# Performance work log

Hardware: AMD Instinct MI355X
Metric: run time of the kernel (lower is better)

## Reference

```python
import jax, jax.numpy as jnp
import numpy as np

B, L, N, F = 8, 4096, 128, 128          # batch, pixels (64x64), memories, filters
H, DK, DV = 8, 16, 32                   # heads, key dim/head, value dim/head
TK, TV = H * DK, H * DV                 # total key depth 128, total value depth 256
BOT, FFN = 256, 2048                    # bottleneck (2*filters), feed-forward channels
EPS = 1e-3                              # keras BatchNormalization epsilon
INV = float(1.0 / np.sqrt(1.0 + EPS))   # inference BN with moving mean=0, var=1


def _bn_pair(k, shape):
    kg, kb = jax.random.split(k)
    gamma = jax.random.uniform(kg, shape, jnp.float32, 0.5, 1.5)
    beta = 0.1 * jax.random.normal(kb, shape, jnp.float32)
    return jnp.stack([gamma, beta])


def setup_inputs() -> dict:
    key = jax.random.key(0)
    ks = jax.random.split(key, 24)
    s = float(BOT) ** -0.5  # TruncatedNormal(stddev=bottleneck**-0.5) init for qkv convs
    return {
        "pixel_input": jax.random.normal(ks[0], (B, L, F), jnp.float32),
        "memory_input": jax.random.normal(ks[1], (B, N, F), jnp.float32),
        "W_mem1": 0.05 * jax.random.normal(ks[2], (F, BOT), jnp.float32),
        "bn_mem1": _bn_pair(ks[3], (BOT,)),
        "W_pix1": 0.05 * jax.random.normal(ks[4], (F, BOT), jnp.float32),
        "bn_pix1": _bn_pair(ks[5], (BOT,)),
        "W_mem_qkv": s * jax.random.normal(ks[6], (BOT, 2 * TK + TV), jnp.float32),
        "bn_mem_qkv": _bn_pair(ks[7], (2 * TK + TV,)),
        "W_pix_qkv": s * jax.random.normal(ks[8], (BOT, 2 * TK + TV), jnp.float32),
        "bn_pix_qkv": _bn_pair(ks[9], (2 * TK + TV,)),
        "bn_mem_sim": _bn_pair(ks[10], (H,)),
        "bn_mem_ret": _bn_pair(ks[11], (H, DV)),
        "bn_pix_sim": _bn_pair(ks[12], (H,)),
        "bn_pix_ret": _bn_pair(ks[13], (H, DV)),
        "W_mem3": 0.05 * jax.random.normal(ks[14], (TV, F), jnp.float32),
        "bn_mem3": _bn_pair(ks[15], (F,)),
        "W_pix3": 0.05 * jax.random.normal(ks[16], (TV, F), jnp.float32),
        "bn_pix3": _bn_pair(ks[17], (F,)),
        "W_ffn1": 0.05 * jax.random.normal(ks[18], (F, FFN), jnp.float32),
        "bn_ffn1": _bn_pair(ks[19], (FFN,)),
        "W_ffn2": 0.05 * jax.random.normal(ks[20], (FFN, F), jnp.float32),
        "bn_ffn2": _bn_pair(ks[21], (F,)),
    }


def _cbn(x, W, p, relu=False):
    """Conv1D (kernel=1) + inference BatchNorm over channels (+ optional relu)."""
    y = jnp.einsum('blc,cd->bld', x, W)
    y = y * (p[0] * INV) + p[1]
    return jax.nn.relu(y) if relu else y


def _heads(t, d):
    b, l, _ = t.shape  # [b, l, H*d] -> [b, H, l, d]
    return t.reshape(b, l, H, d).transpose(0, 2, 1, 3)


def reference(pixel_input, memory_input, W_mem1, bn_mem1, W_pix1, bn_pix1,
              W_mem_qkv, bn_mem_qkv, W_pix_qkv, bn_pix_qkv,
              bn_mem_sim, bn_mem_ret, bn_pix_sim, bn_pix_ret,
              W_mem3, bn_mem3, W_pix3, bn_pix3,
              W_ffn1, bn_ffn1, W_ffn2, bn_ffn2):
    # Bottleneck projections (conv1 + BN + relu)
    mem = _cbn(memory_input, W_mem1, bn_mem1, True)   # [B, N, BOT]
    pix = _cbn(pixel_input, W_pix1, bn_pix1, True)    # [B, L, BOT]

    # QKV projections (conv + BN, no activation)
    mqkv = _cbn(mem, W_mem_qkv, bn_mem_qkv)           # [B, N, 2*TK+TV]
    pqkv = _cbn(pix, W_pix_qkv, bn_pix_qkv)           # [B, L, 2*TK+TV]
    mq, mk, mv = mqkv[..., :TK], mqkv[..., TK:2 * TK], mqkv[..., 2 * TK:]
    pq, pk, pv = pqkv[..., :TK], pqkv[..., TK:2 * TK], pqkv[..., 2 * TK:]
    mq_h, mk_h = _heads(mq, DK), _heads(mk, DK)       # [B, H, N, DK]
    pq_h, pk_h = _heads(pq, DK), _heads(pk, DK)       # [B, H, L, DK]
    mv_h = mv.reshape(B, N, H, DV)                    # [B, N, H, DV]
    pv_h = pv.reshape(B, L, H, DV)                    # [B, L, H, DV]

    # Memory path: memory2pixel attention + memory self-attention share softmax
    k_cat = jnp.concatenate([pk_h, mk_h], axis=2)     # [B, H, L+N, DK]
    v_cat = jnp.concatenate([pv_h, mv_h], axis=1)     # [B, L+N, H, DV]
    logits = jnp.einsum('bhnd,bhmd->bhnm', mq_h, k_cat)
    logits = logits * (bn_mem_sim[0] * INV)[None, :, None, None] + bn_mem_sim[1][None, :, None, None]
    attn = jax.nn.softmax(logits, axis=-1)
    ret = jnp.einsum('bhnm,bmhd->bhnd', attn, v_cat)  # [B, H, N, DV]
    ret = ret * (bn_mem_ret[0] * INV)[None, :, None, :] + bn_mem_ret[1][None, :, None, :]
    ret = jax.nn.relu(ret).transpose(0, 2, 1, 3).reshape(B, N, TV)
    mem_out = jax.nn.relu(memory_input + _cbn(ret, W_mem3, bn_mem3))
    ffn = _cbn(mem_out, W_ffn1, bn_ffn1, True)
    mem_out = jax.nn.relu(mem_out + _cbn(ffn, W_ffn2, bn_ffn2))

    # Pixel path: pixel2memory feedback attention (sigmoid activation)
    plogits = jnp.einsum('bhld,bhnd->bhln', pq_h, mk_h)
    plogits = plogits * (bn_pix_sim[0] * INV)[None, :, None, None] + bn_pix_sim[1][None, :, None, None]
    pattn = jax.nn.sigmoid(plogits)
    pret = jnp.einsum('bhln,bnhd->bhld', pattn, mv_h)  # [B, H, L, DV]
    pret = pret * (bn_pix_ret[0] * INV)[None, :, None, :] + bn_pix_ret[1][None, :, None, :]
    pret = jax.nn.relu(pret).transpose(0, 2, 1, 3).reshape(B, L, TV)
    pix_out = jax.nn.relu(pixel_input + _cbn(pret, W_pix3, bn_pix3))

    return pix_out, mem_out
```

## Files before the change

kernel.cpp:

```cpp
#include <hip/hip_runtime.h>

typedef __attribute__((ext_vector_type(8))) short short8;
typedef __attribute__((ext_vector_type(4))) float floatx4;

#define INVC 0.9995003746877732f
#define NCHUNK 33

__device__ __forceinline__ unsigned short f2bf(float f) {
    union { float f; unsigned int u; } c; c.f = f;
    unsigned int r = c.u + 0x7fffu + ((c.u >> 16) & 1u);
    return (unsigned short)(r >> 16);
}
__device__ __forceinline__ unsigned int f2bf2(float a, float b) {
    return (unsigned int)f2bf(a) | ((unsigned int)f2bf(b) << 16);
}
__device__ __forceinline__ float bf2f(unsigned short u) {
    union { unsigned int u; float f; } c; c.u = ((unsigned int)u) << 16;
    return c.f;
}
__device__ __forceinline__ void gld_lds16(const unsigned short* g, unsigned short* l) {
    __builtin_amdgcn_global_load_lds(
        (const __attribute__((address_space(1))) unsigned int*)g,
        (__attribute__((address_space(3))) unsigned int*)l, 16, 0, 0);
}
__device__ __forceinline__ int fidx(int row, int k) {
    return (k >> 5) * 512 + (row + 16 * ((k >> 3) & 3)) * 8 + (k & 7);
}

struct PrepPtrs {
    const float* src_pix;
    unsigned short* dst_pix;
    const float* W[8]; unsigned short* Wt[8];
};

__global__ __launch_bounds__(256) void prep_kernel(PrepPtrs P) {
    __shared__ float T[32][33];
    const int bid = blockIdx.x, t = threadIdx.x;
    if (bid < 4096) {
        int i = bid * 1024 + t * 4;
        float4 v = *(const float4*)(P.src_pix + i);
        unsigned long long pk = (unsigned long long)f2bf(v.x)
            | ((unsigned long long)f2bf(v.y) << 16)
            | ((unsigned long long)f2bf(v.z) << 32)
            | ((unsigned long long)f2bf(v.w) << 48);
        *(unsigned long long*)(P.dst_pix + i) = pk;
        return;
    }
    int rel = bid - 4096;
    const int KD[8]  = {128,128,256,256,256,256,128,2048};
    const int ND[8]  = {256,256,512,512,128,128,2048,128};
    const int CNT[8] = {32,32,128,128,32,32,256,256};
    int wi = 0;
    #pragma unroll
    for (int k = 0; k < 8; ++k) { if (rel >= CNT[k] && wi == k) { rel -= CNT[k]; wi = k + 1; } }
    const int K = KD[wi], N = ND[wi];
    const int ntn = N >> 5;
    const int tn = rel % ntn, tk = rel / ntn;
    const int n0 = tn * 32, k0 = tk * 32;
    const float* W = P.W[wi];
    unsigned short* Wt = P.Wt[wi];
    const int tx = t & 31, ty = t >> 5;
    #pragma unroll
    for (int i = 0; i < 4; ++i)
        T[ty + 8*i][tx] = W[(size_t)(k0 + ty + 8*i) * N + n0 + tx];
    __syncthreads();
    #pragma unroll
    for (int i = 0; i < 4; ++i)
        Wt[(size_t)(n0 + ty + 8*i) * K + k0 + tx] = f2bf(T[tx][ty + 8*i]);
}

__device__ __forceinline__ void gemm_body(
    const unsigned short* __restrict__ A,
    const unsigned short* __restrict__ Bt,
    const float* __restrict__ bnp,
    const float* __restrict__ residF,
    float* __restrict__ outF,
    int K, int Nc, int row0, int col0,
    unsigned short* As, unsigned short* Bs)
{
    const int t = threadIdx.x;
    const int lane = t & 63, w = t >> 6;
    const int l15 = lane & 15, quad = lane >> 4;
    const int wr = w >> 1, wc = w & 1;

    floatx4 acc[4][4];
    #pragma unroll
    for (int i = 0; i < 4; ++i)
        #pragma unroll
        for (int j = 0; j < 4; ++j) acc[i][j] = (floatx4){0.f, 0.f, 0.f, 0.f};

    const unsigned short* gA0 = A  + (size_t)(row0 + w*16     + l15) * K + quad*8;
    const unsigned short* gA1 = A  + (size_t)(row0 + (w+4)*16 + l15) * K + quad*8;
    const unsigned short* gB0 = Bt + (size_t)(col0 + w*16     + l15) * K + quad*8;
    const unsigned short* gB1 = Bt + (size_t)(col0 + (w+4)*16 + l15) * K + quad*8;
    unsigned short* lA0 = &As[w * 512];
    unsigned short* lA1 = &As[(w + 4) * 512];
    unsigned short* lB0 = &Bs[w * 512];
    unsigned short* lB1 = &Bs[(w + 4) * 512];

    for (int k0 = 0; k0 < K; k0 += 32) {
        __syncthreads();
        gld_lds16(gA0 + k0, lA0);
        gld_lds16(gA1 + k0, lA1);
        gld_lds16(gB0 + k0, lB0);
        gld_lds16(gB1 + k0, lB1);
        __syncthreads();
        short8 a[4], b[4];
        #pragma unroll
        for (int mt = 0; mt < 4; ++mt) a[mt] = *(const short8*)&As[(wr*4 + mt)*512 + lane*8];
        #pragma unroll
        for (int nt = 0; nt < 4; ++nt) b[nt] = *(const short8*)&Bs[(wc*4 + nt)*512 + lane*8];
        #pragma unroll
        for (int mt = 0; mt < 4; ++mt)
            #pragma unroll
            for (int nt = 0; nt < 4; ++nt)
                acc[mt][nt] = __builtin_amdgcn_mfma_f32_16x16x32_bf16(a[mt], b[nt], acc[mt][nt], 0, 0, 0);
    }

    #pragma unroll
    for (int mt = 0; mt < 4; ++mt) {
        const int rowb = row0 + wr*64 + mt*16 + quad*4;
        #pragma unroll
        for (int nt = 0; nt < 4; ++nt) {
            const int col = col0 + wc*64 + nt*16 + l15;
            floatx4 v = acc[mt][nt];
            const float g  = bnp[col] * INVC;
            const float be = bnp[Nc + col];
            #pragma unroll
            for (int r = 0; r < 4; ++r) {
                size_t off = (size_t)(rowb + r) * Nc + col;
                float v1 = v[r] * g + be + residF[off];
                outF[off] = fmaxf(v1, 0.f);
            }
        }
    }
}

__global__ __launch_bounds__(256) void k_qkv(
    const unsigned short* __restrict__ pixB,
    const unsigned short* __restrict__ Wt1, const float* __restrict__ bn1,
    const unsigned short* __restrict__ Wt2, const float* __restrict__ bnq,
    unsigned short* __restrict__ pqkvB,
    const float* __restrict__ memory_input,
    const unsigned short* __restrict__ Wm0, const float* __restrict__ bnm1,
    const unsigned short* __restrict__ Wm2, const float* __restrict__ bnmq,
    unsigned short* __restrict__ mqkv)
{
    __shared__ unsigned short A2[64*512];
    const int t = threadIdx.x;
    const int lane = t & 63, w = t >> 6;
    const int l15 = lane & 15, quad = lane >> 4;

    if (blockIdx.x < 256) {
        const int row0 = blockIdx.x * 128;
        short8 afr[4][4];
        float ga[4][4], ba[4][4];
        #pragma unroll
        for (int i = 0; i < 4; ++i) {
            #pragma unroll
            for (int kc = 0; kc < 4; ++kc)
                afr[i][kc] = *(const short8*)&Wt1[(size_t)(w*64 + i*16 + l15)*128 + kc*32 + quad*8];
            #pragma unroll
            for (int r = 0; r < 4; ++r) {
                const int col = w*64 + i*16 + quad*4 + r;
                ga[i][r] = bn1[col] * INVC;
                ba[i][r] = bn1[256 + col];
            }
        }
        #pragma unroll
        for (int ru = 0; ru < 8; ++ru) {
            short8 bfr[4];
            #pragma unroll
            for (int kc = 0; kc < 4; ++kc)
                bfr[kc] = *(const short8*)&pixB[(size_t)(row0 + ru*16 + l15)*128 + kc*32 + quad*8];
            #pragma unroll
            for (int i = 0; i < 4; ++i) {
                floatx4 acc = {0.f,0.f,0.f,0.f};
                #pragma unroll
                for (int kc = 0; kc < 4; ++kc)
                    acc = __builtin_amdgcn_mfma_f32_16x16x32_bf16(afr[i][kc], bfr[kc], acc, 0, 0, 0);
                float v[4];
                #pragma unroll
                for (int r = 0; r < 4; ++r)
                    v[r] = fmaxf(acc[r]*ga[i][r] + ba[i][r], 0.f);
                const int unit = ru*8 + w*2 + (i >> 1);
                const int koff = (i & 1)*2 + (quad >> 1);
                const int off  = unit*512 + (l15 + 16*koff)*8 + (quad & 1)*4;
                uint2 pk; pk.x = f2bf2(v[0], v[1]); pk.y = f2bf2(v[2], v[3]);
                *(uint2*)&A2[off] = pk;
            }
        }
        __syncthreads();

        #pragma unroll
        for (int op = 0; op < 4; ++op) {
            short8 a0[8], a1[8];
            float g2[2][4], b2[2][4];
            #pragma unroll
            for (int kc = 0; kc < 8; ++kc) {
                a0[kc] = *(const short8*)&Wt2[(size_t)(w*128 + (op*2+0)*16 + l15)*256 + kc*32 + quad*8];
                a1[kc] = *(const short8*)&Wt2[(size_t)(w*128 + (op*2+1)*16 + l15)*256 + kc*32 + quad*8];
            }
            #pragma unroll
            for (int e = 0; e < 2; ++e)
                #pragma unroll
                for (int r = 0; r < 4; ++r) {
                    const int col = w*128 + (op*2+e)*16 + quad*4 + r;
                    g2[e][r] = bnq[col] * INVC;
                    b2[e][r] = bnq[512 + col];
                }
            #pragma unroll
            for (int ru = 0; ru < 8; ++ru) {
                short8 b[8];
                #pragma unroll
                for (int kc = 0; kc < 8; ++kc)
                    b[kc] = *(const short8*)&A2[(ru*8 + kc)*512 + lane*8];
                floatx4 acc0 = {0.f,0.f,0.f,0.f}, acc1 = {0.f,0.f,0.f,0.f};
                #pragma unroll
                for (int kc = 0; kc < 8; ++kc) {
                    acc0 = __builtin_amdgcn_mfma_f32_16x16x32_bf16(a0[kc], b[kc], acc0, 0, 0, 0);
                    acc1 = __builtin_amdgcn_mfma_f32_16x16x32_bf16(a1[kc], b[kc], acc1, 0, 0, 0);
                }
                const int row = row0 + ru*16 + l15;
                unsigned long long pk0 =
                    (unsigned long long)f2bf2(acc0[0]*g2[0][0]+b2[0][0], acc0[1]*g2[0][1]+b2[0][1])
                  | ((unsigned long long)f2bf2(acc0[2]*g2[0][2]+b2[0][2], acc0[3]*g2[0][3]+b2[0][3]) << 32);
                unsigned long long pk1 =
                    (unsigned long long)f2bf2(acc1[0]*g2[1][0]+b2[1][0], acc1[1]*g2[1][1]+b2[1][1])
                  | ((unsigned long long)f2bf2(acc1[2]*g2[1][2]+b2[1][2], acc1[3]*g2[1][3]+b2[1][3]) << 32);
                *(unsigned long long*)&pqkvB[(size_t)row*512 + w*128 + (op*2+0)*16 + quad*4] = pk0;
                *(unsigned long long*)&pqkvB[(size_t)row*512 + w*128 + (op*2+1)*16 + quad*4] = pk1;
            }
        }
        return;
    }

    unsigned short* A0 = &A2[0];
    unsigned short* A1 = &A2[4*512];
    const int g0 = (blockIdx.x - 256) * 16;
    {
        const int row = t >> 4;
        const int c0 = (t & 15) * 8;
        const float* src = memory_input + (size_t)(g0 + row) * 128 + c0;
        float4 v0 = *(const float4*)src;
        float4 v1 = *(const float4*)(src + 4);
        float vv[8] = {v0.x, v0.y, v0.z, v0.w, v1.x, v1.y, v1.z, v1.w};
        #pragma unroll
        for (int e = 0; e < 8; ++e)
            A0[fidx(row, c0 + e)] = f2bf(vv[e]);
    }
    __syncthreads();
    #pragma unroll
    for (int i = 0; i < 4; ++i) {
        const int n0 = (w*4 + i) * 16;
        floatx4 acc = {0.f,0.f,0.f,0.f};
        #pragma unroll
        for (int kc = 0; kc < 4; ++kc) {
            short8 a = *(const short8*)&A0[kc*512 + lane*8];
            short8 bfr = *(const short8*)&Wm0[(size_t)(n0 + l15)*128 + kc*32 + quad*8];
            acc = __builtin_amdgcn_mfma_f32_16x16x32_bf16(a, bfr, acc, 0, 0, 0);
        }
        const int col = n0 + l15;
        const float g = bnm1[col] * INVC, be = bnm1[256 + col];
        #pragma unroll
        for (int r = 0; r < 4; ++r)
            A1[fidx(quad*4 + r, col)] = f2bf(fmaxf(acc[r]*g + be, 0.f));
    }
    __syncthreads();
    #pragma unroll
    for (int i = 0; i < 8; ++i) {
        const int n0 = w*128 + i*16;
        floatx4 acc = {0.f,0.f,0.f,0.f};
        #pragma unroll
        for (int kc = 0; kc < 8; ++kc) {
            short8 a = *(const short8*)&A1[kc*512 + lane*8];
            short8 bfr = *(const short8*)&Wm2[(size_t)(n0 + l15)*256 + kc*32 + quad*8];
            acc = __builtin_amdgcn_mfma_f32_16x16x32_bf16(a, bfr, acc, 0, 0, 0);
        }
        const int col = n0 + l15;
        const float g = bnmq[col] * INVC, be = bnmq[512 + col];
        #pragma unroll
        for (int r = 0; r < 4; ++r)
            mqkv[(size_t)(g0 + quad*4 + r)*512 + col] = f2bf(acc[r]*g + be);
    }
}

__global__ __launch_bounds__(256, 4) void k_attn(
    const unsigned short* __restrict__ pqkv,
    const unsigned short* __restrict__ mqkv,
    const float* __restrict__ bn_psim, const float* __restrict__ bn_pret,
    unsigned short* __restrict__ pret,
    const float* __restrict__ bn_msim,
    float* __restrict__ part_acc, float* __restrict__ part_ml)
{
    __shared__ unsigned short Qs[4*512];
    __shared__ unsigned short Ks[8*512];
    __shared__ unsigned short VsT[8*512];
    __shared__ unsigned short Ps[16*512];
    const int t = threadIdx.x;
    const int lane = t & 63, w = t >> 6;
    const int l15 = lane & 15, quad = lane >> 4;
    floatx4 z4 = {0.f, 0.f, 0.f, 0.f};
    const uint4 zz = make_uint4(0u,0u,0u,0u);

    const int is_pix = (blockIdx.x < 4096);
    int b, h, qrow0, c = 0, qh = 0;
    const unsigned short* kvbase;
    if (is_pix) {
        const int bx = blockIdx.x;
        const int lt = bx & 63; h = (bx >> 6) & 7; b = bx >> 9;
        qrow0 = b*4096 + lt*64;
        kvbase = mqkv + ((size_t)(b*128) << 9);
    } else {
        const int bxm = blockIdx.x - 4096;
        c = bxm % NCHUNK;
        const int rest = bxm / NCHUNK;
        qh = rest & 1; h = (rest >> 1) & 7; b = rest >> 4;
        qrow0 = b*128 + qh*64;
        kvbase = (c < 32) ? (pqkv + ((size_t)(b*4096 + c*128) << 9))
                          : (mqkv + ((size_t)(b*128) << 9));
    }
    const unsigned short* qbase = is_pix ? pqkv : mqkv;

    {
        const int r = t >> 1, half = t & 1;
        if (t < 128) {
            const unsigned short* src = qbase + ((size_t)(qrow0 + r) << 9) + h*16 + half*8;
            *(uint4*)&Qs[(r>>4)*512 + ((r&15) + 16*half)*8] = *(const uint4*)src;
            *(uint4*)&Qs[(r>>4)*512 + ((r&15) + 16*(2+half))*8] = zz;
        }
        const unsigned short* ksrc = kvbase + ((size_t)r << 9) + 128 + h*16 + half*8;
        *(uint4*)&Ks[(r>>4)*512 + ((r&15) + 16*half)*8] = *(const uint4*)ksrc;
        *(uint4*)&Ks[(r>>4)*512 + ((r&15) + 16*(2+half))*8] = zz;
        const unsigned short* vsrc = kvbase + ((size_t)r << 9) + 256 + h*32 + half*16;
        uint4 va = *(const uint4*)vsrc;
        uint4 vb = *(const uint4*)(vsrc + 8);
        unsigned short ev[16] = {
            (unsigned short)(va.x & 0xffffu), (unsigned short)(va.x >> 16),
            (unsigned short)(va.y & 0xffffu), (unsigned short)(va.y >> 16),
            (unsigned short)(va.z & 0xffffu), (unsigned short)(va.z >> 16),
            (unsigned short)(va.w & 0xffffu), (unsigned short)(va.w >> 16),
            (unsigned short)(vb.x & 0xffffu), (unsigned short)(vb.x >> 16),
            (unsigned short)(vb.y & 0xffffu), (unsigned short)(vb.y >> 16),
            (unsigned short)(vb.z & 0xffffu), (unsigned short)(vb.z >> 16),
            (unsigned short)(vb.w & 0xffffu), (unsigned short)(vb.w >> 16)};
        const int vbase_off = (half*4 + (r>>5))*512 + 16*((r>>3)&3)*8 + (r&7);
        #pragma unroll
        for (int e = 0; e < 16; ++e)
            VsT[vbase_off + e*8] = ev[e];
    }
    __syncthreads();

    const float simg = (is_pix ? bn_psim[h] : bn_msim[h]) * INVC;
    const float simb =  is_pix ? bn_psim[8 + h] : bn_msim[8 + h];
    short8 bq = *(const short8*)&Qs[w*512 + lane*8];
    float mstat, lstat;

    if (is_pix) {
        #pragma unroll
        for (int nt = 0; nt < 8; ++nt) {
            short8 ak = *(const short8*)&Ks[nt*512 + lane*8];
            floatx4 s = __builtin_amdgcn_mfma_f32_16x16x32_bf16(ak, bq, z4, 0, 0, 0);
            float p[4];
            #pragma unroll
            for (int r = 0; r < 4; ++r) {
                float x = s[r] * simg + simb;
                p[r] = __builtin_amdgcn_rcpf(1.f + __expf(-x));
            }
            const int off = (w*4 + (nt>>1))*512
                          + (l15 + 16*((nt&1)*2 + (quad>>1)))*8 + (quad&1)*4;
            uint2 pk; pk.x = f2bf2(p[0], p[1]); pk.y = f2bf2(p[2], p[3]);
            *(uint2*)&Ps[off] = pk;
        }
    } else {
        floatx4 sv[8];
        float mx = -1e30f;
        #pragma unroll
        for (int nt = 0; nt < 8; ++nt) {
            short8 ak = *(const short8*)&Ks[nt*512 + lane*8];
            floatx4 s = __builtin_amdgcn_mfma_f32_16x16x32_bf16(ak, bq, z4, 0, 0, 0);
            #pragma unroll
            for (int r = 0; r < 4; ++r) {
                sv[nt][r] = s[r] * simg + simb;
                mx = fmaxf(mx, sv[nt][r]);
            }
        }
        mx = fmaxf(mx, __shfl_xor(mx, 16));
        mx = fmaxf(mx, __shfl_xor(mx, 32));
        float lsum = 0.f;
        #pragma unroll
        for (int nt = 0; nt < 8; ++nt) {
            float p[4];
            #pragma unroll
            for (int r = 0; r < 4; ++r) {
                p[r] = __expf(sv[nt][r] - mx);
                lsum += p[r];
            }
            const int off = (w*4 + (nt>>1))*512
                          + (l15 + 16*((nt&1)*2 + (quad>>1)))*8 + (quad&1)*4;
            uint2 pk; pk.x = f2bf2(p[0], p[1]); pk.y = f2bf2(p[2], p[3]);
            *(uint2*)&Ps[off] = pk;
        }
        lsum += __shfl_xor(lsum, 16);
        lsum += __shfl_xor(lsum, 32);
        mstat = mx; lstat = lsum;
    }

    #pragma unroll
    for (int dvt = 0; dvt < 2; ++dvt) {
        floatx4 acc = {0.f,0.f,0.f,0.f};
        #pragma unroll
        for (int ks = 0; ks < 4; ++ks) {
            short8 av = *(const short8*)&VsT[(dvt*4 + ks)*512 + lane*8];
            short8 bp = *(const short8*)&Ps[(w*4 + ks)*512 + lane*8];
            acc = __builtin_amdgcn_mfma_f32_16x16x32_bf16(av, bp, acc, 0, 0, 0);
        }
        if (is_pix) {
            const int q = qrow0 + w*16 + l15;
            float v[4];
            #pragma unroll
            for (int r = 0; r < 4; ++r) {
                const int dv = dvt*16 + quad*4 + r;
                v[r] = fmaxf(acc[r] * (bn_pret[h*32 + dv]*INVC) + bn_pret[256 + h*32 + dv], 0.f);
            }
            unsigned long long pk = (unsigned long long)f2bf2(v[0], v[1])
                                  | ((unsigned long long)f2bf2(v[2], v[3]) << 32);
            *(unsigned long long*)&pret[((size_t)q << 8) + h*32 + dvt*16 + quad*4] = pk;
        } else {
            const int bh = b*8 + h;
            const int q = qh*64 + w*16 + l15;
            float4 st = make_float4(acc[0], acc[1], acc[2], acc[3]);
            *(float4*)&part_acc[((size_t)(bh*NCHUNK + c)*128 + q)*32 + dvt*16 + quad*4] = st;
        }
    }
    if (!is_pix && quad == 0) {
        const int bh = b*8 + h;
        const int q = qh*64 + w*16 + l15;
        size_t o = ((size_t)(bh*NCHUNK + c)*128 + q) * 2;
        float2 ml = make_float2(mstat, lstat);
        *(float2*)&part_ml[o] = ml;
    }
}

__global__ __launch_bounds__(256) void k_pix3_combmem3(
    const unsigned short* __restrict__ pretB, const unsigned short* __restrict__ Wt5,
    const float* __restrict__ bn_pix3, const float* __restrict__ pixel_input,
    float* __restrict__ out_pix,
    const float* __restrict__ part_acc, const float* __restrict__ part_ml,
    const float* __restrict__ bn_ret,
    const unsigned short* __restrict__ Wt4, const float* __restrict__ bn3,
    const float* __restrict__ memory_input,
    unsigned short* __restrict__ moB)
{
    __shared__ unsigned short As[8 * 512];
    __shared__ unsigned short Bs[8 * 512];
    const int bx = blockIdx.x;
    if (bx < 256) {
        gemm_body(pretB, Wt5, bn_pix3, pixel_input, out_pix, 256, 128,
                  bx * 128, 0, As, Bs);
        return;
    }
    unsigned short* mretA = As;
    const int t = threadIdx.x;
    const int lane = t & 63, w = t >> 6;
    const int l15 = lane & 15, quad = lane >> 4;
    const int g0 = (bx - 256) * 16;
    const int b = g0 >> 7;
    const int nbase = g0 & 127;

    {
        const int row = t >> 4;
        const int c0 = (t & 15) * 16;
        const int h = c0 >> 5;
        const int n = nbase + row;
        const int bh = b*8 + h;
        float m_g = -1e30f;
        for (int s = 0; s < NCHUNK; ++s)
            m_g = fmaxf(m_g, part_ml[((size_t)(bh*NCHUNK + s)*128 + n)*2]);
        float l_g = 0.f;
        float og[16];
        #pragma unroll
        for (int e = 0; e < 16; ++e) og[e] = 0.f;
        for (int s = 0; s < NCHUNK; ++s) {
            size_t o = ((size_t)(bh*NCHUNK + s)*128 + n)*2;
            float wgt = __expf(part_ml[o] - m_g);
            l_g += part_ml[o+1] * wgt;
            const float* pa = part_acc + ((size_t)(bh*NCHUNK + s)*128 + n)*32 + (c0 & 31);
            #pragma unroll
            for (int e = 0; e < 16; e += 4) {
                float4 v = *(const float4*)(pa + e);
                og[e]   += v.x*wgt; og[e+1] += v.y*wgt;
                og[e+2] += v.z*wgt; og[e+3] += v.w*wgt;
            }
        }
        float invl = __builtin_amdgcn_rcpf(l_g);
        #pragma unroll
        for (int e = 0; e < 16; ++e) {
            int col = c0 + e;
            int dv = col & 31;
            float v = og[e]*invl*(bn_ret[h*32+dv]*INVC) + bn_ret[256 + h*32 + dv];
            mretA[fidx(row, col)] = f2bf(fmaxf(v, 0.f));
        }
    }
    __syncthreads();

    #pragma unroll
    for (int i = 0; i < 2; ++i) {
        const int n0 = (w*2 + i) * 16;
        floatx4 acc = {0.f,0.f,0.f,0.f};
        #pragma unroll
        for (int kc = 0; kc < 8; ++kc) {
            short8 a = *(const short8*)&mretA[kc*512 + lane*8];
            short8 bfr = *(const short8*)&Wt4[(size_t)(n0 + l15)*256 + kc*32 + quad*8];
            acc = __builtin_amdgcn_mfma_f32_16x16x32_bf16(a, bfr, acc, 0, 0, 0);
        }
        const int col = n0 + l15;
        const float g = bn3[col]*INVC, be = bn3[128 + col];
        #pragma unroll
        for (int r = 0; r < 4; ++r) {
            const int row = quad*4 + r;
            float v = acc[r]*g + be + memory_input[(size_t)(g0 + row)*128 + col];
            moB[(size_t)(g0 + row)*128 + col] = f2bf(fmaxf(v, 0.f));
        }
    }
}

__global__ __launch_bounds__(1024) void k_ffn(
    const unsigned short* __restrict__ moB,
    const unsigned short* __restrict__ Wt6, const float* __restrict__ bnf1,
    const unsigned short* __restrict__ Wt7, const float* __restrict__ bnf2,
    float* __restrict__ out_mem)
{
    __shared__ unsigned short moA[4*512];
    __shared__ unsigned short fA[64*512];
    __shared__ floatx4 red[2][8][64];
    const int t = threadIdx.x;
    const int lane = t & 63, w = t >> 6;
    const int l15 = lane & 15, quad = lane >> 4;
    const int g0 = blockIdx.x * 16;

    if (t < 256) {
        const int row = t >> 4;
        const int c0 = (t & 15) * 8;
        uint4 v = *(const uint4*)(moB + (size_t)(g0 + row)*128 + c0);
        unsigned short ev[8] = {
            (unsigned short)(v.x & 0xffffu), (unsigned short)(v.x >> 16),
            (unsigned short)(v.y & 0xffffu), (unsigned short)(v.y >> 16),
            (unsigned short)(v.z & 0xffffu), (unsigned short)(v.z >> 16),
            (unsigned short)(v.w & 0xffffu), (unsigned short)(v.w >> 16)};
        #pragma unroll
        for (int e = 0; e < 8; ++e) moA[fidx(row, c0+e)] = ev[e];
    }
    __syncthreads();

    #pragma unroll
    for (int i = 0; i < 8; ++i) {
        const int n0 = (w*8 + i) * 16;
        floatx4 acc = {0.f,0.f,0.f,0.f};
        #pragma unroll
        for (int kc = 0; kc < 4; ++kc) {
            short8 a = *(const short8*)&moA[kc*512 + lane*8];
            short8 bfr = *(const short8*)&Wt6[(size_t)(n0 + l15)*128 + kc*32 + quad*8];
            acc = __builtin_amdgcn_mfma_f32_16x16x32_bf16(a, bfr, acc, 0, 0, 0);
        }
        const int col = n0 + l15;
        const float g = bnf1[col]*INVC, be = bnf1[2048 + col];
        #pragma unroll
        for (int r = 0; r < 4; ++r)
            fA[fidx(quad*4 + r, col)] = f2bf(fmaxf(acc[r]*g + be, 0.f));
    }
    __syncthreads();

    {
        const int ntile = w & 7, khalf = w >> 3;
        const int n0 = ntile * 16;
        floatx4 acc = {0.f,0.f,0.f,0.f};
        #pragma unroll 8
        for (int kc = 0; kc < 32; ++kc) {
            const int kcu = khalf*32 + kc;
            short8 a = *(const short8*)&fA[kcu*512 + lane*8];
            short8 bfr = *(const short8*)&Wt7[(size_t)(n0 + l15)*2048 + kcu*32 + quad*8];
            acc = __builtin_amdgcn_mfma_f32_16x16x32_bf16(a, bfr, acc, 0, 0, 0);
        }
        red[khalf][ntile][lane] = acc;
    }
    __syncthreads();
    if (w < 8) {
        const int n0 = w * 16;
        floatx4 s0 = red[0][w][lane];
        floatx4 s1 = red[1][w][lane];
        const int col = n0 + l15;
        const float g = bnf2[col]*INVC, be = bnf2[128 + col];
        #pragma unroll
        for (int r = 0; r < 4; ++r) {
            const int row = quad*4 + r;
            float resid = bf2f(moA[fidx(row, col)]);
            float v = fmaxf((s0[r] + s1[r])*g + be + resid, 0.f);
            out_mem[(size_t)(g0 + row)*128 + col] = v;
        }
    }
}

extern "C" void kernel_launch(void* const* d_in, const int* in_sizes, int n_in,
                              void* d_out, int out_size, void* d_ws, size_t ws_size,
                              hipStream_t stream) {
    const float* pixel_input  = (const float*)d_in[0];
    const float* memory_input = (const float*)d_in[1];
    const float* W_mem1    = (const float*)d_in[2];
    const float* bn_mem1   = (const float*)d_in[3];
    const float* W_pix1    = (const float*)d_in[4];
    const float* bn_pix1   = (const float*)d_in[5];
    const float* W_mem_qkv = (const float*)d_in[6];
    const float* bn_mem_qkv= (const float*)d_in[7];
    const float* W_pix_qkv = (const float*)d_in[8];
    const float* bn_pix_qkv= (const float*)d_in[9];
    const float* bn_mem_sim= (const float*)d_in[10];
    const float* bn_mem_ret= (const float*)d_in[11];
    const float* bn_pix_sim= (const float*)d_in[12];
    const float* bn_pix_ret= (const float*)d_in[13];
    const float* W_mem3    = (const float*)d_in[14];
    const float* bn_mem3   = (const float*)d_in[15];
    const float* W_pix3    = (const float*)d_in[16];
    const float* bn_pix3   = (const float*)d_in[17];
    const float* W_ffn1    = (const float*)d_in[18];
    const float* bn_ffn1   = (const float*)d_in[19];
    const float* W_ffn2    = (const float*)d_in[20];
    const float* bn_ffn2   = (const float*)d_in[21];

    char* ws = (char*)d_ws;
    size_t off = 0;
    auto alloc = [&](size_t bytes) -> void* {
        void* p = ws + off; off += (bytes + 255) & ~(size_t)255; return p;
    };
    unsigned short* pixB  = (unsigned short*)alloc((size_t)32768*128*2);
    unsigned short* Wt0   = (unsigned short*)alloc((size_t)256*128*2);
    unsigned short* Wt1   = (unsigned short*)alloc((size_t)256*128*2);
    unsigned short* Wt2   = (unsigned short*)alloc((size_t)512*256*2);
    unsigned short* Wt3   = (unsigned short*)alloc((size_t)512*256*2);
    unsigned short* Wt4   = (unsigned short*)alloc((size_t)128*256*2);
    unsigned short* Wt5   = (unsigned short*)alloc((size_t)128*256*2);
    unsigned short* Wt6   = (unsigned short*)alloc((size_t)2048*128*2);
    unsigned short* Wt7   = (unsigned short*)alloc((size_t)128*2048*2);
    unsigned short* mqkvB = (unsigned short*)alloc((size_t)1024*512*2);
    unsigned short* pqkvB = (unsigned short*)alloc((size_t)32768*512*2);
    float* part_acc = (float*)alloc((size_t)64*NCHUNK*128*32*4);
    float* part_ml  = (float*)alloc((size_t)64*NCHUNK*128*2*4);
    unsigned short* pretB = (unsigned short*)alloc((size_t)32768*256*2);
    unsigned short* moB   = (unsigned short*)alloc((size_t)1024*128*2);

    float* out_pix = (float*)d_out;
    float* out_mem = (float*)d_out + (size_t)8*4096*128;

    PrepPtrs P;
    P.src_pix = pixel_input;
    P.dst_pix = pixB;
    P.W[0]=W_mem1; P.W[1]=W_pix1; P.W[2]=W_mem_qkv; P.W[3]=W_pix_qkv;
    P.W[4]=W_mem3; P.W[5]=W_pix3; P.W[6]=W_ffn1;    P.W[7]=W_ffn2;
    P.Wt[0]=Wt0; P.Wt[1]=Wt1; P.Wt[2]=Wt2; P.Wt[3]=Wt3;
    P.Wt[4]=Wt4; P.Wt[5]=Wt5; P.Wt[6]=Wt6; P.Wt[7]=Wt7;

    dim3 blk(256);
    prep_kernel<<<4992, blk, 0, stream>>>(P);
    k_qkv<<<320, blk, 0, stream>>>(pixB, Wt1, bn_pix1, Wt3, bn_pix_qkv, pqkvB,
        memory_input, Wt0, bn_mem1, Wt2, bn_mem_qkv, mqkvB);
    k_attn<<<4096 + 128*NCHUNK, blk, 0, stream>>>(pqkvB, mqkvB,
        bn_pix_sim, bn_pix_ret, pretB, bn_mem_sim, part_acc, part_ml);
    k_pix3_combmem3<<<320, blk, 0, stream>>>(pretB, Wt5, bn_pix3, pixel_input, out_pix,
        part_acc, part_ml, bn_mem_ret, Wt4, bn_mem3, memory_input, moB);
    k_ffn<<<64, dim3(1024), 0, stream>>>(moB, Wt6, bn_ffn1, Wt7, bn_ffn2, out_mem);
}
```

Before: 238.1 us.

## Emit Q/K/V in attention-ready tiled layouts and load via direct-to-LDS

The QKV projection kernel now writes queries, keys and transposed values straight into per-head, MFMA-fragment-ordered buffers instead of a row-major [rows,512] array. The V section is computed with swapped operands so it comes out already transposed. The attention kernel then loads each tile with global_load_lds 16-byte copies instead of scattered loads, per-element transposes and shuffles. The aim is to cut global-load inefficiency and LDS transpose work in attention. The cost is more complex index math and scattered writes in the projection kernel.

```diff
diff --git a/kernel.cpp b/kernel.cpp
--- a/kernel.cpp
+++ b/kernel.cpp
@@ -13,6 +13,9 @@
 }
 __device__ __forceinline__ unsigned int f2bf2(float a, float b) {
     return (unsigned int)f2bf(a) | ((unsigned int)f2bf(b) << 16);
+}
+__device__ __forceinline__ unsigned long long pack4(float v0, float v1, float v2, float v3) {
+    return (unsigned long long)f2bf2(v0, v1) | ((unsigned long long)f2bf2(v2, v3) << 32);
 }
 __device__ __forceinline__ float bf2f(unsigned short u) {
     union { unsigned int u; float f; } c; c.u = ((unsigned int)u) << 16;
@@ -39,10 +42,7 @@
     if (bid < 4096) {
         int i = bid * 1024 + t * 4;
         float4 v = *(const float4*)(P.src_pix + i);
-        unsigned long long pk = (unsigned long long)f2bf(v.x)
-            | ((unsigned long long)f2bf(v.y) << 16)
-            | ((unsigned long long)f2bf(v.z) << 32)
-            | ((unsigned long long)f2bf(v.w) << 48);
+        unsigned long long pk = pack4(v.x, v.y, v.z, v.w);
         *(unsigned long long*)(P.dst_pix + i) = pk;
         return;
     }
@@ -140,11 +140,13 @@
     const unsigned short* __restrict__ pixB,
     const unsigned short* __restrict__ Wt1, const float* __restrict__ bn1,
     const unsigned short* __restrict__ Wt2, const float* __restrict__ bnq,
-    unsigned short* __restrict__ pqkvB,
+    unsigned short* __restrict__ qip, unsigned short* __restrict__ kip,
+    unsigned short* __restrict__ vtp,
     const float* __restrict__ memory_input,
     const unsigned short* __restrict__ Wm0, const float* __restrict__ bnm1,
     const unsigned short* __restrict__ Wm2, const float* __restrict__ bnmq,
-    unsigned short* __restrict__ mqkv)
+    unsigned short* __restrict__ qim, unsigned short* __restrict__ kim,
+    unsigned short* __restrict__ vtm)
 {
     __shared__ unsigned short A2[64*512];
     const int t = threadIdx.x;
@@ -153,83 +155,130 @@
 
     if (blockIdx.x < 256) {
         const int row0 = blockIdx.x * 128;
-        short8 afr[4][4];
-        float ga[4][4], ba[4][4];
-        #pragma unroll
-        for (int i = 0; i < 4; ++i) {
-            #pragma unroll
-            for (int kc = 0; kc < 4; ++kc)
-                afr[i][kc] = *(const short8*)&Wt1[(size_t)(w*64 + i*16 + l15)*128 + kc*32 + quad*8];
-            #pragma unroll
-            for (int r = 0; r < 4; ++r) {
-                const int col = w*64 + i*16 + quad*4 + r;
-                ga[i][r] = bn1[col] * INVC;
-                ba[i][r] = bn1[256 + col];
-            }
-        }
-        #pragma unroll
-        for (int ru = 0; ru < 8; ++ru) {
-            short8 bfr[4];
-            #pragma unroll
-            for (int kc = 0; kc < 4; ++kc)
-                bfr[kc] = *(const short8*)&pixB[(size_t)(row0 + ru*16 + l15)*128 + kc*32 + quad*8];
+        const int bb = row0 >> 12;
+        const int runit0 = row0 >> 4;
+        {
+            short8 afr[4][4];
+            float ga[4][4], ba[4][4];
             #pragma unroll
             for (int i = 0; i < 4; ++i) {
-                floatx4 acc = {0.f,0.f,0.f,0.f};
                 #pragma unroll
                 for (int kc = 0; kc < 4; ++kc)
-                    acc = __builtin_amdgcn_mfma_f32_16x16x32_bf16(afr[i][kc], bfr[kc], acc, 0, 0, 0);
-                float v[4];
-                #pragma unroll
-                for (int r = 0; r < 4; ++r)
-                    v[r] = fmaxf(acc[r]*ga[i][r] + ba[i][r], 0.f);
-                const int unit = ru*8 + w*2 + (i >> 1);
-                const int koff = (i & 1)*2 + (quad >> 1);
-                const int off  = unit*512 + (l15 + 16*koff)*8 + (quad & 1)*4;
-                uint2 pk; pk.x = f2bf2(v[0], v[1]); pk.y = f2bf2(v[2], v[3]);
-                *(uint2*)&A2[off] = pk;
+                    afr[i][kc] = *(const short8*)&Wt1[(size_t)(w*64 + i*16 + l15)*128 + kc*32 + quad*8];
+                #pragma unroll
+                for (int r = 0; r < 4; ++r) {
+                    const int col = w*64 + i*16 + quad*4 + r;
+                    ga[i][r] = bn1[col] * INVC;
+                    ba[i][r] = bn1[256 + col];
+                }
+            }
+            #pragma unroll
+            for (int ru = 0; ru < 8; ++ru) {
+                short8 bfr[4];
+                #pragma unroll
+                for (int kc = 0; kc < 4; ++kc)
+                    bfr[kc] = *(const short8*)&pixB[(size_t)(row0 + ru*16 + l15)*128 + kc*32 + quad*8];
+                #pragma unroll
+                for (int i = 0; i < 4; ++i) {
+                    floatx4 acc = {0.f,0.f,0.f,0.f};
+                    #pragma unroll
+                    for (int kc = 0; kc < 4; ++kc)
+                        acc = __builtin_amdgcn_mfma_f32_16x16x32_bf16(afr[i][kc], bfr[kc], acc, 0, 0, 0);
+                    float v[4];
+                    #pragma unroll
+                    for (int r = 0; r < 4; ++r)
+                        v[r] = fmaxf(acc[r]*ga[i][r] + ba[i][r], 0.f);
+                    const int unit = ru*8 + w*2 + (i >> 1);
+                    const int koff = (i & 1)*2 + (quad >> 1);
+                    const int off  = unit*512 + (l15 + 16*koff)*8 + (quad & 1)*4;
+                    uint2 pk; pk.x = f2bf2(v[0], v[1]); pk.y = f2bf2(v[2], v[3]);
+                    *(uint2*)&A2[off] = pk;
+                }
             }
         }
         __syncthreads();
 
-        #pragma unroll
-        for (int op = 0; op < 4; ++op) {
-            short8 a0[8], a1[8];
-            float g2[2][4], b2[2][4];
-            #pragma unroll
-            for (int kc = 0; kc < 8; ++kc) {
-                a0[kc] = *(const short8*)&Wt2[(size_t)(w*128 + (op*2+0)*16 + l15)*256 + kc*32 + quad*8];
-                a1[kc] = *(const short8*)&Wt2[(size_t)(w*128 + (op*2+1)*16 + l15)*256 + kc*32 + quad*8];
-            }
-            #pragma unroll
-            for (int e = 0; e < 2; ++e)
-                #pragma unroll
-                for (int r = 0; r < 4; ++r) {
-                    const int col = w*128 + (op*2+e)*16 + quad*4 + r;
-                    g2[e][r] = bnq[col] * INVC;
-                    b2[e][r] = bnq[512 + col];
+        if (w < 2) {
+            const int sec = w * 128;
+            unsigned short* img = (w == 0) ? qip : kip;
+            const int soff = (l15 + 16*(quad>>1))*8 + (quad&1)*4;
+            for (int op = 0; op < 4; ++op) {
+                short8 a0[8], a1[8];
+                float g2[2][4], be2[2][4];
+                #pragma unroll
+                for (int kc = 0; kc < 8; ++kc) {
+                    a0[kc] = *(const short8*)&Wt2[(size_t)(sec + (op*2+0)*16 + l15)*256 + kc*32 + quad*8];
+                    a1[kc] = *(const short8*)&Wt2[(size_t)(sec + (op*2+1)*16 + l15)*256 + kc*32 + quad*8];
                 }
-            #pragma unroll
-            for (int ru = 0; ru < 8; ++ru) {
-                short8 b[8];
-                #pragma unroll
-                for (int kc = 0; kc < 8; ++kc)
-                    b[kc] = *(const short8*)&A2[(ru*8 + kc)*512 + lane*8];
-                floatx4 acc0 = {0.f,0.f,0.f,0.f}, acc1 = {0.f,0.f,0.f,0.f};
+                #pragma unroll
+                for (int e = 0; e < 2; ++e)
+                    #pragma unroll
+                    for (int r = 0; r < 4; ++r) {
+                        const int col = sec + (op*2+e)*16 + quad*4 + r;
+                        g2[e][r] = bnq[col]*INVC; be2[e][r] = bnq[512+col];
+                    }
+                #pragma unroll
+                for (int ru = 0; ru < 8; ++ru) {
+                    short8 bv[8];
+                    #pragma unroll
+                    for (int kc = 0; kc < 8; ++kc)
+                        bv[kc] = *(const short8*)&A2[(ru*8+kc)*512 + lane*8];
+                    floatx4 acc0 = {0.f,0.f,0.f,0.f}, acc1 = {0.f,0.f,0.f,0.f};
+                    #pragma unroll
+                    for (int kc = 0; kc < 8; ++kc) {
+                        acc0 = __builtin_amdgcn_mfma_f32_16x16x32_bf16(a0[kc], bv[kc], acc0, 0, 0, 0);
+                        acc1 = __builtin_amdgcn_mfma_f32_16x16x32_bf16(a1[kc], bv[kc], acc1, 0, 0, 0);
+                    }
+                    unsigned long long pk0 = pack4(acc0[0]*g2[0][0]+be2[0][0], acc0[1]*g2[0][1]+be2[0][1],
+                                                  acc0[2]*g2[0][2]+be2[0][2], acc0[3]*g2[0][3]+be2[0][3]);
+                    unsigned long long pk1 = pack4(acc1[0]*g2[1][0]+be2[1][0], acc1[1]*g2[1][1]+be2[1][1],
+                                                  acc1[2]*g2[1][2]+be2[1][2], acc1[3]*g2[1][3]+be2[1][3]);
+                    *(unsigned long long*)&img[(size_t)((runit0+ru)*8 + op*2+0)*256 + soff] = pk0;
+                    *(unsigned long long*)&img[(size_t)((runit0+ru)*8 + op*2+1)*256 + soff] = pk1;
+                }
+            }
+        } else {
+            const int dvb = (w-2)*128;
+            for (int op = 0; op < 4; ++op) {
+                short8 b0[8], b1[8];
+                const int dvg0 = dvb + (op*2+0)*16 + l15;
+                const int dvg1 = dvb + (op*2+1)*16 + l15;
                 #pragma unroll
                 for (int kc = 0; kc < 8; ++kc) {
-                    acc0 = __builtin_amdgcn_mfma_f32_16x16x32_bf16(a0[kc], b[kc], acc0, 0, 0, 0);
-                    acc1 = __builtin_amdgcn_mfma_f32_16x16x32_bf16(a1[kc], b[kc], acc1, 0, 0, 0);
+                    b0[kc] = *(const short8*)&Wt2[(size_t)(256 + dvg0)*256 + kc*32 + quad*8];
+                    b1[kc] = *(const short8*)&Wt2[(size_t)(256 + dvg1)*256 + kc*32 + quad*8];
                 }
-                const int row = row0 + ru*16 + l15;
-                unsigned long long pk0 =
-                    (unsigned long long)f2bf2(acc0[0]*g2[0][0]+b2[0][0], acc0[1]*g2[0][1]+b2[0][1])
-                  | ((unsigned long long)f2bf2(acc0[2]*g2[0][2]+b2[0][2], acc0[3]*g2[0][3]+b2[0][3]) << 32);
-                unsigned long long pk1 =
-                    (unsigned long long)f2bf2(acc1[0]*g2[1][0]+b2[1][0], acc1[1]*g2[1][1]+b2[1][1])
-                  | ((unsigned long long)f2bf2(acc1[2]*g2[1][2]+b2[1][2], acc1[3]*g2[1][3]+b2[1][3]) << 32);
-                *(unsigned long long*)&pqkvB[(size_t)row*512 + w*128 + (op*2+0)*16 + quad*4] = pk0;
-                *(unsigned long long*)&pqkvB[(size_t)row*512 + w*128 + (op*2+1)*16 + quad*4] = pk1;
+                const float gv0 = bnq[256 + dvg0]*INVC, bv0 = bnq[512 + 256 + dvg0];
+                const float gv1 = bnq[256 + dvg1]*INVC, bv1 = bnq[512 + 256 + dvg1];
+                const int h0 = dvg0 >> 5, dv16_0 = dvg0 & 15, du0 = (dvg0 >> 4) & 1;
+                const int h1 = dvg1 >> 5, dv16_1 = dvg1 & 15, du1 = (dvg1 >> 4) & 1;
+                #pragma unroll
+                for (int ru = 0; ru < 8; ++ru) {
+                    short8 av[8];
+                    #pragma unroll
+                    for (int kc = 0; kc < 8; ++kc)
+                        av[kc] = *(const short8*)&A2[(ru*8+kc)*512 + lane*8];
+                    floatx4 acc0 = {0.f,0.f,0.f,0.f}, acc1 = {0.f,0.f,0.f,0.f};
+                    #pragma unroll
+                    for (int kc = 0; kc < 8; ++kc) {
+                        acc0 = __builtin_amdgcn_mfma_f32_16x16x32_bf16(av[kc], b0[kc], acc0, 0, 0, 0);
+                        acc1 = __builtin_amdgcn_mfma_f32_16x16x32_bf16(av[kc], b1[kc], acc1, 0, 0, 0);
+                    }
+                    const int keyb = (row0 & 4095) + ru*16 + quad*4;
+                    const int kcv = keyb >> 5;
+                    const int g3 = (keyb >> 3) & 3;
+                    const int jb = (quad & 1)*4;
+                    unsigned long long pk0 = pack4(acc0[0]*gv0+bv0, acc0[1]*gv0+bv0,
+                                                  acc0[2]*gv0+bv0, acc0[3]*gv0+bv0);
+                    unsigned long long pk1 = pack4(acc1[0]*gv1+bv1, acc1[1]*gv1+bv1,
+                                                  acc1[2]*gv1+bv1, acc1[3]*gv1+bv1);
+                    size_t u0 = (size_t)((bb*8 + h0)*256 + (kcv>>2)*8 + du0*4 + (kcv&3))*512
+                              + (dv16_0 + 16*g3)*8 + jb;
+                    size_t u1 = (size_t)((bb*8 + h1)*256 + (kcv>>2)*8 + du1*4 + (kcv&3))*512
+                              + (dv16_1 + 16*g3)*8 + jb;
+                    *(unsigned long long*)&vtp[u0] = pk0;
+                    *(unsigned long long*)&vtp[u1] = pk1;
+                }
             }
         }
         return;
@@ -238,6 +287,7 @@
     unsigned short* A0 = &A2[0];
     unsigned short* A1 = &A2[4*512];
     const int g0 = (blockIdx.x - 256) * 16;
+    const int bb = g0 >> 7, ru = (g0 >> 4) & 7;
     {
         const int row = t >> 4;
         const int c0 = (t & 15) * 8;
@@ -267,27 +317,88 @@
             A1[fidx(quad*4 + r, col)] = f2bf(fmaxf(acc[r]*g + be, 0.f));
     }
     __syncthreads();
-    #pragma unroll
-    for (int i = 0; i < 8; ++i) {
-        const int n0 = w*128 + i*16;
-        floatx4 acc = {0.f,0.f,0.f,0.f};
-        #pragma unroll
-        for (int kc = 0; kc < 8; ++kc) {
-            short8 a = *(const short8*)&A1[kc*512 + lane*8];
-            short8 bfr = *(const short8*)&Wm2[(size_t)(n0 + l15)*256 + kc*32 + quad*8];
-            acc = __builtin_amdgcn_mfma_f32_16x16x32_bf16(a, bfr, acc, 0, 0, 0);
-        }
-        const int col = n0 + l15;
-        const float g = bnmq[col] * INVC, be = bnmq[512 + col];
-        #pragma unroll
-        for (int r = 0; r < 4; ++r)
-            mqkv[(size_t)(g0 + quad*4 + r)*512 + col] = f2bf(acc[r]*g + be);
+    if (w < 2) {
+        const int sec = w * 128;
+        unsigned short* img = (w == 0) ? qim : kim;
+        const int soff = (l15 + 16*(quad>>1))*8 + (quad&1)*4;
+        for (int op = 0; op < 4; ++op) {
+            short8 a0[8], a1f[8];
+            float g2[2][4], be2[2][4];
+            #pragma unroll
+            for (int kc = 0; kc < 8; ++kc) {
+                a0[kc]  = *(const short8*)&Wm2[(size_t)(sec + (op*2+0)*16 + l15)*256 + kc*32 + quad*8];
+                a1f[kc] = *(const short8*)&Wm2[(size_t)(sec + (op*2+1)*16 + l15)*256 + kc*32 + quad*8];
+            }
+            #pragma unroll
+            for (int e = 0; e < 2; ++e)
+                #pragma unroll
+                for (int r = 0; r < 4; ++r) {
+                    const int col = sec + (op*2+e)*16 + quad*4 + r;
+                    g2[e][r] = bnmq[col]*INVC; be2[e][r] = bnmq[512+col];
+                }
+            short8 bv[8];
+            #pragma unroll
+            for (int kc = 0; kc < 8; ++kc)
+                bv[kc] = *(const short8*)&A1[kc*512 + lane*8];
+            floatx4 acc0 = {0.f,0.f,0.f,0.f}, acc1 = {0.f,0.f,0.f,0.f};
+            #pragma unroll
+            for (int kc = 0; kc < 8; ++kc) {
+                acc0 = __builtin_amdgcn_mfma_f32_16x16x32_bf16(a0[kc],  bv[kc], acc0, 0, 0, 0);
+                acc1 = __builtin_amdgcn_mfma_f32_16x16x32_bf16(a1f[kc], bv[kc], acc1, 0, 0, 0);
+            }
+            unsigned long long pk0 = pack4(acc0[0]*g2[0][0]+be2[0][0], acc0[1]*g2[0][1]+be2[0][1],
+                                          acc0[2]*g2[0][2]+be2[0][2], acc0[3]*g2[0][3]+be2[0][3]);
+            unsigned long long pk1 = pack4(acc1[0]*g2[1][0]+be2[1][0], acc1[1]*g2[1][1]+be2[1][1],
+                                          acc1[2]*g2[1][2]+be2[1][2], acc1[3]*g2[1][3]+be2[1][3]);
+            *(unsigned long long*)&img[(size_t)((bb*8+ru)*8 + op*2+0)*256 + soff] = pk0;
+            *(unsigned long long*)&img[(size_t)((bb*8+ru)*8 + op*2+1)*256 + soff] = pk1;
+        }
+    } else {
+        const int dvb = (w-2)*128;
+        for (int op = 0; op < 4; ++op) {
+            short8 b0[8], b1[8];
+            const int dvg0 = dvb + (op*2+0)*16 + l15;
+            const int dvg1 = dvb + (op*2+1)*16 + l15;
+            #pragma unroll
+            for (int kc = 0; kc < 8; ++kc) {
+                b0[kc] = *(const short8*)&Wm2[(size_t)(256 + dvg0)*256 + kc*32 + quad*8];
+                b1[kc] = *(const short8*)&Wm2[(size_t)(256 + dvg1)*256 + kc*32 + quad*8];
+            }
+            const float gv0 = bnmq[256 + dvg0]*INVC, bv0 = bnmq[512 + 256 + dvg0];
+            const float gv1 = bnmq[256 + dvg1]*INVC, bv1 = bnmq[512 + 256 + dvg1];
+            const int h0 = dvg0 >> 5, dv16_0 = dvg0 & 15, du0 = (dvg0 >> 4) & 1;
+            const int h1 = dvg1 >> 5, dv16_1 = dvg1 & 15, du1 = (dvg1 >> 4) & 1;
+            short8 av[8];
+            #pragma unroll
+            for (int kc = 0; kc < 8; ++kc)
+                av[kc] = *(const short8*)&A1[kc*512 + lane*8];
+            floatx4 acc0 = {0.f,0.f,0.f,0.f}, acc1 = {0.f,0.f,0.f,0.f};
+            #pragma unroll
+            for (int kc = 0; kc < 8; ++kc) {
+                acc0 = __builtin_amdgcn_mfma_f32_16x16x32_bf16(av[kc], b0[kc], acc0, 0, 0, 0);
+                acc1 = __builtin_amdgcn_mfma_f32_16x16x32_bf16(av[kc], b1[kc], acc1, 0, 0, 0);
+            }
+            const int keyb = (g0 & 127) + quad*4;
+            const int kcv = keyb >> 5;
+            const int g3 = (keyb >> 3) & 3;
+            const int jb = (quad & 1)*4;
+            unsigned long long pk0 = pack4(acc0[0]*gv0+bv0, acc0[1]*gv0+bv0,
+                                          acc0[2]*gv0+bv0, acc0[3]*gv0+bv0);
+            unsigned long long pk1 = pack4(acc1[0]*gv1+bv1, acc1[1]*gv1+bv1,
+                                          acc1[2]*gv1+bv1, acc1[3]*gv1+bv1);
+            size_t u0 = (size_t)((bb*8 + h0)*8 + du0*4 + kcv)*512 + (dv16_0 + 16*g3)*8 + jb;
+            size_t u1 = (size_t)((bb*8 + h1)*8 + du1*4 + kcv)*512 + (dv16_1 + 16*g3)*8 + jb;
+            *(unsigned long long*)&vtm[u0] = pk0;
+            *(unsigned long long*)&vtm[u1] = pk1;
+        }
     }
 }
 
 __global__ __launch_bounds__(256, 4) void k_attn(
-    const unsigned short* __restrict__ pqkv,
-    const unsigned short* __restrict__ mqkv,
+    const unsigned short* __restrict__ qip, const unsigned short* __restrict__ kip,
+    const unsigned short* __restrict__ vtp,
+    const unsigned short* __restrict__ qim, const unsigned short* __restrict__ kim,
+    const unsigned short* __restrict__ vtm,
     const float* __restrict__ bn_psim, const float* __restrict__ bn_pret,
     unsigned short* __restrict__ pret,
     const float* __restrict__ bn_msim,
@@ -301,54 +412,48 @@
     const int lane = t & 63, w = t >> 6;
     const int l15 = lane & 15, quad = lane >> 4;
     floatx4 z4 = {0.f, 0.f, 0.f, 0.f};
-    const uint4 zz = make_uint4(0u,0u,0u,0u);
 
     const int is_pix = (blockIdx.x < 4096);
     int b, h, qrow0, c = 0, qh = 0;
-    const unsigned short* kvbase;
+    const unsigned short *qsrc, *ksrc0, *ksrc1, *vsrc0, *vsrc1;
     if (is_pix) {
         const int bx = blockIdx.x;
         const int lt = bx & 63; h = (bx >> 6) & 7; b = bx >> 9;
         qrow0 = b*4096 + lt*64;
-        kvbase = mqkv + ((size_t)(b*128) << 9);
+        qsrc  = qip + (size_t)((b*256 + lt*4 + w)*8 + h)*256;
+        ksrc0 = kim + (size_t)((b*8 + w)*8 + h)*256;
+        ksrc1 = kim + (size_t)((b*8 + w+4)*8 + h)*256;
+        vsrc0 = vtm + (size_t)((b*8+h)*8 + w)*512;
+        vsrc1 = vtm + (size_t)((b*8+h)*8 + w+4)*512;
     } else {
         const int bxm = blockIdx.x - 4096;
         c = bxm % NCHUNK;
         const int rest = bxm / NCHUNK;
         qh = rest & 1; h = (rest >> 1) & 7; b = rest >> 4;
         qrow0 = b*128 + qh*64;
-        kvbase = (c < 32) ? (pqkv + ((size_t)(b*4096 + c*128) << 9))
-                          : (mqkv + ((size_t)(b*128) << 9));
-    }
-    const unsigned short* qbase = is_pix ? pqkv : mqkv;
-
-    {
-        const int r = t >> 1, half = t & 1;
-        if (t < 128) {
-            const unsigned short* src = qbase + ((size_t)(qrow0 + r) << 9) + h*16 + half*8;
-            *(uint4*)&Qs[(r>>4)*512 + ((r&15) + 16*half)*8] = *(const uint4*)src;
-            *(uint4*)&Qs[(r>>4)*512 + ((r&15) + 16*(2+half))*8] = zz;
-        }
-        const unsigned short* ksrc = kvbase + ((size_t)r << 9) + 128 + h*16 + half*8;
-        *(uint4*)&Ks[(r>>4)*512 + ((r&15) + 16*half)*8] = *(const uint4*)ksrc;
-        *(uint4*)&Ks[(r>>4)*512 + ((r&15) + 16*(2+half))*8] = zz;
-        const unsigned short* vsrc = kvbase + ((size_t)r << 9) + 256 + h*32 + half*16;
-        uint4 va = *(const uint4*)vsrc;
-        uint4 vb = *(const uint4*)(vsrc + 8);
-        unsigned short ev[16] = {
-            (unsigned short)(va.x & 0xffffu), (unsigned short)(va.x >> 16),
-            (unsigned short)(va.y & 0xffffu), (unsigned short)(va.y >> 16),
-            (unsigned short)(va.z & 0xffffu), (unsigned short)(va.z >> 16),
-            (unsigned short)(va.w & 0xffffu), (unsigned short)(va.w >> 16),
-            (unsigned short)(vb.x & 0xffffu), (unsigned short)(vb.x >> 16),
-            (unsigned short)(vb.y & 0xffffu), (unsigned short)(vb.y >> 16),
-            (unsigned short)(vb.z & 0xffffu), (unsigned short)(vb.z >> 16),
-            (unsigned short)(vb.w & 0xffffu), (unsigned short)(vb.w >> 16)};
-        const int vbase_off = (half*4 + (r>>5))*512 + 16*((r>>3)&3)*8 + (r&7);
-        #pragma unroll
-        for (int e = 0; e < 16; ++e)
-            VsT[vbase_off + e*8] = ev[e];
-    }
+        qsrc = qim + (size_t)((b*8 + qh*4 + w)*8 + h)*256;
+        if (c < 32) {
+            ksrc0 = kip + (size_t)((b*256 + c*8 + w)*8 + h)*256;
+            ksrc1 = kip + (size_t)((b*256 + c*8 + w+4)*8 + h)*256;
+            vsrc0 = vtp + (size_t)((b*8+h)*256 + c*8 + w)*512;
+            vsrc1 = vtp + (size_t)((b*8+h)*256 + c*8 + w+4)*512;
+        } else {
+            ksrc0 = kim + (size_t)((b*8 + w)*8 + h)*256;
+            ksrc1 = kim + (size_t)((b*8 + w+4)*8 + h)*256;
+            vsrc0 = vtm + (size_t)((b*8+h)*8 + w)*512;
+            vsrc1 = vtm + (size_t)((b*8+h)*8 + w+4)*512;
+        }
+    }
+
+    if (lane < 32) {
+        gld_lds16(qsrc  + lane*8, &Qs[w*512]);
+        gld_lds16(ksrc0 + lane*8, &Ks[w*512]);
+        gld_lds16(ksrc1 + lane*8, &Ks[(w+4)*512]);
+    }
+    gld_lds16(vsrc0 + lane*8, &VsT[w*512]);
+    gld_lds16(vsrc1 + lane*8, &VsT[(w+4)*512]);
+    *(uint2*)&Qs[(t>>6)*512 + 256 + (t&63)*4] = make_uint2(0u, 0u);
+    *(uint4*)&Ks[(t>>5)*512 + 256 + (t&31)*8] = make_uint4(0u,0u,0u,0u);
     __syncthreads();
 
     const float simg = (is_pix ? bn_psim[h] : bn_msim[h]) * INVC;
@@ -423,9 +528,8 @@
                 const int dv = dvt*16 + quad*4 + r;
                 v[r] = fmaxf(acc[r] * (bn_pret[h*32 + dv]*INVC) + bn_pret[256 + h*32 + dv], 0.f);
             }
-            unsigned long long pk = (unsigned long long)f2bf2(v[0], v[1])
-                                  | ((unsigned long long)f2bf2(v[2], v[3]) << 32);
-            *(unsigned long long*)&pret[((size_t)q << 8) + h*32 + dvt*16 + quad*4] = pk;
+            *(unsigned long long*)&pret[((size_t)q << 8) + h*32 + dvt*16 + quad*4]
+                = pack4(v[0], v[1], v[2], v[3]);
         } else {
             const int bh = b*8 + h;
             const int q = qh*64 + w*16 + l15;
@@ -437,8 +541,7 @@
         const int bh = b*8 + h;
         const int q = qh*64 + w*16 + l15;
         size_t o = ((size_t)(bh*NCHUNK + c)*128 + q) * 2;
-        float2 ml = make_float2(mstat, lstat);
-        *(float2*)&part_ml[o] = ml;
+        *(float2*)&part_ml[o] = make_float2(mstat, lstat);
     }
 }
 
@@ -641,8 +744,12 @@
     unsigned short* Wt5   = (unsigned short*)alloc((size_t)128*256*2);
     unsigned short* Wt6   = (unsigned short*)alloc((size_t)2048*128*2);
     unsigned short* Wt7   = (unsigned short*)alloc((size_t)128*2048*2);
-    unsigned short* mqkvB = (unsigned short*)alloc((size_t)1024*512*2);
-    unsigned short* pqkvB = (unsigned short*)alloc((size_t)32768*512*2);
+    unsigned short* qip   = (unsigned short*)alloc((size_t)2048*8*256*2);
+    unsigned short* kip   = (unsigned short*)alloc((size_t)2048*8*256*2);
+    unsigned short* vtp   = (unsigned short*)alloc((size_t)64*256*512*2);
+    unsigned short* qim   = (unsigned short*)alloc((size_t)64*8*256*2);
+    unsigned short* kim   = (unsigned short*)alloc((size_t)64*8*256*2);
+    unsigned short* vtm   = (unsigned short*)alloc((size_t)64*8*512*2);
     float* part_acc = (float*)alloc((size_t)64*NCHUNK*128*32*4);
     float* part_ml  = (float*)alloc((size_t)64*NCHUNK*128*2*4);
     unsigned short* pretB = (unsigned short*)alloc((size_t)32768*256*2);
@@ -661,9 +768,10 @@
 
     dim3 blk(256);
     prep_kernel<<<4992, blk, 0, stream>>>(P);
-    k_qkv<<<320, blk, 0, stream>>>(pixB, Wt1, bn_pix1, Wt3, bn_pix_qkv, pqkvB,
-        memory_input, Wt0, bn_mem1, Wt2, bn_mem_qkv, mqkvB);
-    k_attn<<<4096 + 128*NCHUNK, blk, 0, stream>>>(pqkvB, mqkvB,
+    k_qkv<<<320, blk, 0, stream>>>(pixB, Wt1, bn_pix1, Wt3, bn_pix_qkv,
+        qip, kip, vtp,
+        memory_input, Wt0, bn_mem1, Wt2, bn_mem_qkv, qim, kim, vtm);
+    k_attn<<<4096 + 128*NCHUNK, blk, 0, stream>>>(qip, kip, vtp, qim, kim, vtm,
         bn_pix_sim, bn_pix_ret, pretB, bn_mem_sim, part_acc, part_ml);
     k_pix3_combmem3<<<320, blk, 0, stream>>>(pretB, Wt5, bn_pix3, pixel_input, out_pix,
         part_acc, part_ml, bn_mem_ret, Wt4, bn_mem3, memory_input, moB);
```

Measured after the change: 240.6 us. About the same (+1.0%).
